# Optimization experiments

Measured on AMD Instinct MI355X. Metric: run time of the kernel, lower is better.

## Reference

```python
import jax, jax.numpy as jnp
import numpy as np

B, N, C = 8, 3072, 768
NUM_HEADS, NUM_DIL, KS = 12, 3, 3


def setup_inputs() -> dict:
    key = jax.random.key(0)
    k1, k2, k3 = jax.random.split(key, 3)
    x = jax.random.normal(k1, (B, N, C), dtype=jnp.float32)
    qkv_w = jax.random.normal(k2, (3 * C, C), dtype=jnp.float32) * 0.02
    proj_w = jax.random.normal(k3, (C, C), dtype=jnp.float32) * 0.02
    proj_b = jnp.zeros((C,), dtype=jnp.float32)
    return {"x": x, "qkv_w": qkv_w, "proj_w": proj_w, "proj_b": proj_b}


def reference(x, qkv_w, proj_w, proj_b):
    Bx, Nx, Cx = x.shape
    nd, ks, heads = NUM_DIL, KS, NUM_HEADS
    hd = Cx // heads          # head_dim = 64
    d = Cx // nd              # channels per dilation = 256
    h = heads // nd           # heads per dilation = 4
    nb = Nx // ks             # number of windows along N
    scale = hd ** -0.5

    # qkv: [B,N,3C] -> [nd,3,B,d,N] (matches torch permute(3,2,0,4,1))
    qkv = (x @ qkv_w.T).reshape(Bx, Nx, 3, nd, d)
    qkv = jnp.transpose(qkv, (3, 2, 0, 4, 1))
    q, k, v = qkv[:, 0], qkv[:, 1], qkv[:, 2]  # each [nd,B,d,N]

    def split_heads(t):
        # [nd,B,d,N] -> [nd,B,h,hd,ks,nb] -> [nd,B,h,nb,ks,hd]
        t = t.reshape(nd, Bx, h, hd, ks, nb)
        return jnp.transpose(t, (0, 1, 2, 5, 4, 3))

    qh = split_heads(q)
    kh = split_heads(k)
    vh = split_heads(v)

    # tiny per-window attention: [nd,B,h,nb,ks,ks]
    attn = jnp.einsum('nbhwqd,nbhwkd->nbhwqk', qh, kh) * scale
    attn = jax.nn.softmax(attn, axis=-1)
    out = jnp.einsum('nbhwqk,nbhwkd->nbhwqd', attn, vh)  # [nd,B,h,nb,ks,hd]

    # torch: transpose(1,2).reshape(B,N,d) per dilation, then permute(1,2,0,3).reshape(B,N,C)
    out = jnp.transpose(out, (0, 1, 3, 2, 4, 5)).reshape(nd, Bx, Nx, d)
    out = jnp.transpose(out, (1, 2, 0, 3)).reshape(Bx, Nx, Cx)
    return out @ proj_w.T + proj_b
```

## Files before the change

kernel.cpp:

```cpp
#include <hip/hip_runtime.h>
#include <stdint.h>

#define DEVFN __device__ __forceinline__

typedef unsigned short u16;
typedef __bf16 bf16_t;
typedef bf16_t bf16x8 __attribute__((ext_vector_type(8)));
typedef float  f32x4  __attribute__((ext_vector_type(4)));

static constexpr int Bb = 8, Nn = 3072, Cc = 768;
static constexpr int Mr = Bb * Nn;
static constexpr int C3 = 3 * Cc;
static constexpr int NB = 1024;

DEVFN u16 f2bf_rne(float f) {
  uint32_t u = __builtin_bit_cast(uint32_t, f);
  u += 0x7FFFu + ((u >> 16) & 1u);
  return (u16)(u >> 16);
}
DEVFN float bf2f(u16 v) {
  uint32_t u = ((uint32_t)v) << 16;
  return __builtin_bit_cast(float, u);
}

__global__ void cvt_all(const float4* __restrict__ x, const float4* __restrict__ wq,
                        const float4* __restrict__ wp, ushort4* __restrict__ xb,
                        ushort4* __restrict__ wqb, ushort4* __restrict__ wpb) {
  const int NX = Mr * Cc / 4, NQ = C3 * Cc / 4, NP = Cc * Cc / 4;
  int i = blockIdx.x * blockDim.x + threadIdx.x;
  const int stride = gridDim.x * blockDim.x;
  for (; i < NX + NQ + NP; i += stride) {
    const float4* src; ushort4* dst; int j;
    if (i < NX)           { src = x;  dst = xb;  j = i; }
    else if (i < NX + NQ) { src = wq; dst = wqb; j = i - NX; }
    else                  { src = wp; dst = wpb; j = i - NX - NQ; }
    float4 v = src[j];
    ushort4 o;
    o.x = f2bf_rne(v.x); o.y = f2bf_rne(v.y);
    o.z = f2bf_rne(v.z); o.w = f2bf_rne(v.w);
    dst[j] = o;
  }
}

DEVFN void gload_lds16(const void* g, void* l) {
  __builtin_amdgcn_global_load_lds(
      (const __attribute__((address_space(1))) uint32_t*)g,
      (__attribute__((address_space(3))) uint32_t*)l,
      16, 0, 0);
}

template <int BM, int BN, int WM, int WN, bool OUT_F32>
__global__ __launch_bounds__(WM * WN * 64, 2)
void gemm_bk64(const u16* __restrict__ A, const u16* __restrict__ Bw,
               void* __restrict__ Cout, const float* __restrict__ bias,
               int Ndim, int K) {
  constexpr int NT = WM * WN * 64;
  constexpr int MF = BM / WM / 16;
  constexpr int NF = BN / WN / 16;
  constexpr int SLOT = (BM + BN) * 128;
  static_assert(4 * (NT / 8) == BM && BM == BN, "staging geometry");
  __shared__ char lds[2 * SLOT];

  const int nTn = Ndim / BN;
  const int nwg = gridDim.x;
  const int bid = blockIdx.x;
  const int wgid = (bid & 7) * (nwg >> 3) + (bid >> 3);
  const int tm = wgid / nTn, tn = wgid % nTn;

  const int t = threadIdx.x;
  const int l = t & 63;
  const int w = t >> 6;
  const int wr = w / WN;
  const int wc = w % WN;

  const int NSL = K >> 6;

  const int srA = t >> 3;
  const int sw8 = ((t & 7) ^ ((t >> 3) & 7)) * 8;
  const u16* baseA = A  + (size_t)(tm * BM) * K + sw8;
  const u16* baseB = Bw + (size_t)(tn * BN) * K + sw8;

  const int lt0 = (l & 15) * 128 + (((l >> 4)    ) ^ (l & 7)) * 16;
  const int lt1 = (l & 15) * 128 + (((l >> 4) + 4) ^ (l & 7)) * 16;

  f32x4 acc[MF][NF];
  #pragma unroll
  for (int m = 0; m < MF; ++m)
    #pragma unroll
    for (int n = 0; n < NF; ++n)
      acc[m][n] = f32x4{0.f, 0.f, 0.f, 0.f};

#define STAGE(SL, P)                                                          \
  do {                                                                        \
    char* d = lds + (SL) * SLOT + t * 16;                                     \
    const size_t ko = (size_t)(P) * 64;                                       \
    _Pragma("unroll")                                                         \
    for (int k = 0; k < 4; ++k)                                               \
      gload_lds16(baseA + (size_t)(k * (NT / 8) + srA) * K + ko,              \
                  d + k * NT * 16);                                           \
    _Pragma("unroll")                                                         \
    for (int k = 0; k < 4; ++k)                                               \
      gload_lds16(baseB + (size_t)(k * (NT / 8) + srA) * K + ko,              \
                  d + (k + 4) * NT * 16);                                     \
  } while (0)

  STAGE(0, 0);

  for (int p = 0; p < NSL; ++p) {
    asm volatile("s_waitcnt vmcnt(0)" ::: "memory");
    __builtin_amdgcn_s_barrier();

    const char* ab = lds + (p & 1) * SLOT + wr * (BM / WM) * 128;
    const char* bb = lds + (p & 1) * SLOT + BM * 128 + wc * (BN / WN) * 128;

    bf16x8 af[MF], bf[NF];
    #pragma unroll
    for (int m = 0; m < MF; ++m)
      af[m] = *reinterpret_cast<const bf16x8*>(ab + m * 2048 + lt0);
    #pragma unroll
    for (int n = 0; n < NF; ++n)
      bf[n] = *reinterpret_cast<const bf16x8*>(bb + n * 2048 + lt0);

    if (p + 1 < NSL) STAGE((p + 1) & 1, p + 1);

    __builtin_amdgcn_s_setprio(1);
    #pragma unroll
    for (int m = 0; m < MF; ++m)
      #pragma unroll
      for (int n = 0; n < NF; ++n)
        acc[m][n] = __builtin_amdgcn_mfma_f32_16x16x32_bf16(bf[n], af[m],
                                                            acc[m][n], 0, 0, 0);
    __builtin_amdgcn_s_setprio(0);

    #pragma unroll
    for (int m = 0; m < MF; ++m)
      af[m] = *reinterpret_cast<const bf16x8*>(ab + m * 2048 + lt1);
    #pragma unroll
    for (int n = 0; n < NF; ++n)
      bf[n] = *reinterpret_cast<const bf16x8*>(bb + n * 2048 + lt1);

    __builtin_amdgcn_s_setprio(1);
    #pragma unroll
    for (int m = 0; m < MF; ++m)
      #pragma unroll
      for (int n = 0; n < NF; ++n)
        acc[m][n] = __builtin_amdgcn_mfma_f32_16x16x32_bf16(bf[n], af[m],
                                                            acc[m][n], 0, 0, 0);
    __builtin_amdgcn_s_setprio(0);
  }
#undef STAGE

  const int grow0 = tm * BM + wr * (BM / WM) + (l & 15);
  const int gcol0 = tn * BN + wc * (BN / WN) + (l >> 4) * 4;
  #pragma unroll
  for (int m = 0; m < MF; ++m) {
    const int row = grow0 + m * 16;
    #pragma unroll
    for (int n = 0; n < NF; ++n) {
      const int col = gcol0 + n * 16;
      if constexpr (OUT_F32) {
        float* O = (float*)Cout;
        const float4 bv = *reinterpret_cast<const float4*>(&bias[col]);
        float4 o;
        o.x = acc[m][n][0] + bv.x;
        o.y = acc[m][n][1] + bv.y;
        o.z = acc[m][n][2] + bv.z;
        o.w = acc[m][n][3] + bv.w;
        *reinterpret_cast<float4*>(&O[(size_t)row * Ndim + col]) = o;
      } else {
        u16* O = (u16*)Cout;
        ushort4 o;
        o.x = f2bf_rne(acc[m][n][0]);
        o.y = f2bf_rne(acc[m][n][1]);
        o.z = f2bf_rne(acc[m][n][2]);
        o.w = f2bf_rne(acc[m][n][3]);
        *reinterpret_cast<ushort4*>(&O[(size_t)row * Ndim + col]) = o;
      }
    }
  }
}

__global__ __launch_bounds__(256)
void attn_local4(const u16* __restrict__ qkv, u16* __restrict__ y) {
  const int t = threadIdx.x;
  const int l = t & 63;
  int wid = blockIdx.x * 4 + (t >> 6);
  const int w = wid & (NB - 1); wid >>= 10;
  const int b = wid & 7; wid >>= 3;
  const int dil = wid;

  const int colq = dil * 256 + l * 4;
  float q[3][4], k[3][4], v[3][4];
  #pragma unroll
  for (int i = 0; i < 3; ++i) {
    const size_t row = (size_t)(b * Nn + i * NB + w) * C3;
    const ushort4 q4 = *reinterpret_cast<const ushort4*>(&qkv[row + colq]);
    const ushort4 k4 = *reinterpret_cast<const ushort4*>(&qkv[row + 768 + colq]);
    const ushort4 v4 = *reinterpret_cast<const ushort4*>(&qkv[row + 1536 + colq]);
    q[i][0] = bf2f(q4.x); q[i][1] = bf2f(q4.y); q[i][2] = bf2f(q4.z); q[i][3] = bf2f(q4.w);
    k[i][0] = bf2f(k4.x); k[i][1] = bf2f(k4.y); k[i][2] = bf2f(k4.z); k[i][3] = bf2f(k4.w);
    v[i][0] = bf2f(v4.x); v[i][1] = bf2f(v4.y); v[i][2] = bf2f(v4.z); v[i][3] = bf2f(v4.w);
  }

  float s[3][3];
  #pragma unroll
  for (int i = 0; i < 3; ++i)
    #pragma unroll
    for (int j = 0; j < 3; ++j) {
      float p = q[i][0] * k[j][0] + q[i][1] * k[j][1]
              + q[i][2] * k[j][2] + q[i][3] * k[j][3];
      p += __shfl_xor(p, 1, 64);
      p += __shfl_xor(p, 2, 64);
      p += __shfl_xor(p, 4, 64);
      p += __shfl_xor(p, 8, 64);
      s[i][j] = p * 0.125f;
    }

  #pragma unroll
  for (int i = 0; i < 3; ++i) {
    const float mx = fmaxf(fmaxf(s[i][0], s[i][1]), s[i][2]);
    const float e0 = __expf(s[i][0] - mx);
    const float e1 = __expf(s[i][1] - mx);
    const float e2 = __expf(s[i][2] - mx);
    const float inv = 1.0f / (e0 + e1 + e2);
    ushort4 o4;
    u16* po = &o4.x;
    #pragma unroll
    for (int e = 0; e < 4; ++e)
      po[e] = f2bf_rne((e0 * v[0][e] + e1 * v[1][e] + e2 * v[2][e]) * inv);
    const int linear = (l >> 4) * 192 + i * 64 + (l & 15) * 4;
    const int nout = w * 3 + (linear >> 8);
    const int dd = linear & 255;
    *reinterpret_cast<ushort4*>(
        &y[(size_t)(b * Nn + nout) * Cc + dil * 256 + dd]) = o4;
  }
}

extern "C" void kernel_launch(void* const* d_in, const int* in_sizes, int n_in,
                              void* d_out, int out_size, void* d_ws, size_t ws_size,
                              hipStream_t stream) {
  const float* x      = (const float*)d_in[0];
  const float* qkv_w  = (const float*)d_in[1];
  const float* proj_w = (const float*)d_in[2];
  const float* proj_b = (const float*)d_in[3];

  char* ws = (char*)d_ws;
  u16* wq_b = (u16*)(ws);
  u16* wp_b = (u16*)(ws + 3538944);
  u16* xb   = (u16*)(ws + 4718592);
  u16* qkvb = (u16*)(ws + 42467328);
  u16* yb   = xb;

  cvt_all<<<2048, 256, 0, stream>>>((const float4*)x, (const float4*)qkv_w,
                                    (const float4*)proj_w, (ushort4*)xb,
                                    (ushort4*)wq_b, (ushort4*)wp_b);

  gemm_bk64<256, 256, 2, 4, false>
      <<<(Mr / 256) * (C3 / 256), 512, 0, stream>>>(xb, wq_b, qkvb, nullptr, C3, Cc);

  attn_local4<<<(3 * 8 * 1024) / 4, 256, 0, stream>>>(qkvb, yb);

  gemm_bk64<128, 128, 2, 2, true>
      <<<(Mr / 128) * (Cc / 128), 256, 0, stream>>>(yb, wp_b, d_out, proj_b, Cc, Cc);
}
```

Baseline: 203.2 us.

## Add 4-stage BK32 pipelined 256x256 GEMM for the QKV projection

Adds a dedicated 256x256-tile bf16 GEMM for the QKV projection. It uses K-steps of 32 with a 4-slot LDS ring, prefetching three phases ahead via global_load_lds and fine-grained vmcnt waits. It also uses a swizzled LDS layout and raises wave priority around the MFMA blocks. The goal is to hide global-load latency better than the previous double-buffered BK64 kernel. In exchange it uses 128KB of LDS, which may limit occupancy to one workgroup per CU despite the launch bound of 2.

After: 196.7 us, median of 2. -3.2%, faster.

```diff
diff --git a/kernel.cpp b/kernel.cpp
--- a/kernel.cpp
+++ b/kernel.cpp
@@ -47,6 +47,120 @@
       (const __attribute__((address_space(1))) uint32_t*)g,
       (__attribute__((address_space(3))) uint32_t*)l,
       16, 0, 0);
+}
+
+template <bool OUT_F32>
+__global__ __launch_bounds__(512, 2)
+void gemm256(const u16* __restrict__ A, const u16* __restrict__ Bw,
+             void* __restrict__ Cout, const float* __restrict__ bias,
+             int Ndim, int K) {
+  constexpr int SLOT = 32768;
+  __shared__ char lds[4 * SLOT];
+
+  const int nTn = Ndim >> 8;
+  const int nwg = gridDim.x;
+  const int bid = blockIdx.x;
+  const int wgid = (bid & 7) * (nwg >> 3) + (bid >> 3);
+  const int tm = wgid / nTn, tn = wgid % nTn;
+
+  const int t = threadIdx.x;
+  const int l = t & 63;
+  const int w = t >> 6;
+  const int wr = w >> 2;
+  const int wcq = w & 3;
+  const int lr = l & 15;
+
+  const int NPH = K >> 5;
+
+  const int srow = l >> 2;
+  const int scol = 8 * ((l & 3) ^ (srow & 3));
+  const u16* pA0 = A  + (size_t)(tm * 256 +       w * 16 + srow) * K + scol;
+  const u16* pA1 = A  + (size_t)(tm * 256 + 128 + w * 16 + srow) * K + scol;
+  const u16* pB0 = Bw + (size_t)(tn * 256 +       w * 16 + srow) * K + scol;
+  const u16* pB1 = Bw + (size_t)(tn * 256 + 128 + w * 16 + srow) * K + scol;
+
+  const int lane_off = lr * 64 + (((l >> 4) * 16) ^ ((lr & 3) << 4));
+
+  f32x4 acc[8][4];
+  #pragma unroll
+  for (int m = 0; m < 8; ++m)
+    #pragma unroll
+    for (int n = 0; n < 4; ++n)
+      acc[m][n] = f32x4{0.f, 0.f, 0.f, 0.f};
+
+  #pragma unroll
+  for (int q = 0; q < 3; ++q) {
+    char* dA = &lds[q * SLOT + w * 1024];
+    char* dB = &lds[q * SLOT + 16384 + w * 1024];
+    const size_t ko = (size_t)q * 32;
+    gload_lds16(pA0 + ko, dA);
+    gload_lds16(pA1 + ko, dA + 8192);
+    gload_lds16(pB0 + ko, dB);
+    gload_lds16(pB1 + ko, dB + 8192);
+  }
+
+#define GPHASE(VMSTR, PF_COND)                                                \
+  do {                                                                        \
+    asm volatile(VMSTR ::: "memory");                                         \
+    __builtin_amdgcn_s_barrier();                                             \
+    asm volatile("" ::: "memory");                                            \
+    const char* ab = &lds[(p & 3) * SLOT] + wr * 8192 + lane_off;             \
+    const char* bb = &lds[(p & 3) * SLOT + 16384] + wcq * 4096 + lane_off;    \
+    bf16x8 af[8], bf[4];                                                      \
+    _Pragma("unroll")                                                         \
+    for (int m = 0; m < 8; ++m)                                               \
+      af[m] = *reinterpret_cast<const bf16x8*>(ab + m * 1024);                \
+    _Pragma("unroll")                                                         \
+    for (int n = 0; n < 4; ++n)                                               \
+      bf[n] = *reinterpret_cast<const bf16x8*>(bb + n * 1024);                \
+    if (PF_COND) {                                                            \
+      const int ps = (p + 3) & 3;                                             \
+      char* dA = &lds[ps * SLOT + w * 1024];                                  \
+      char* dB = &lds[ps * SLOT + 16384 + w * 1024];                          \
+      const size_t ko = (size_t)(p + 3) * 32;                                 \
+      gload_lds16(pA0 + ko, dA);                                              \
+      gload_lds16(pA1 + ko, dA + 8192);                                       \
+      gload_lds16(pB0 + ko, dB);                                              \
+      gload_lds16(pB1 + ko, dB + 8192);                                       \
+    }                                                                         \
+    __builtin_amdgcn_s_setprio(1);                                            \
+    _Pragma("unroll")                                                         \
+    for (int m = 0; m < 8; ++m)                                               \
+      _Pragma("unroll")                                                       \
+      for (int n = 0; n < 4; ++n)                                             \
+        acc[m][n] = __builtin_amdgcn_mfma_f32_16x16x32_bf16(af[m], bf[n],     \
+                                                            acc[m][n], 0,0,0);\
+    __builtin_amdgcn_s_setprio(0);                                            \
+    asm volatile("" ::: "memory");                                            \
+  } while (0)
+
+  int p = 0;
+  for (; p < NPH - 2; ++p) GPHASE("s_waitcnt vmcnt(8)", (p + 3 < NPH));
+  GPHASE("s_waitcnt vmcnt(4)", false); ++p;
+  GPHASE("s_waitcnt vmcnt(0)", false); ++p;
+#undef GPHASE
+
+  const int rbase = tm * 256 + wr * 128 + (l >> 4) * 4;
+  #pragma unroll
+  for (int m = 0; m < 8; ++m) {
+    #pragma unroll
+    for (int n = 0; n < 4; ++n) {
+      const int col = tn * 256 + wcq * 64 + n * 16 + lr;
+      const int row0 = rbase + m * 16;
+      if constexpr (OUT_F32) {
+        float* O = (float*)Cout;
+        const float bv = bias[col];
+        #pragma unroll
+        for (int j = 0; j < 4; ++j)
+          O[(size_t)(row0 + j) * Ndim + col] = acc[m][n][j] + bv;
+      } else {
+        u16* O = (u16*)Cout;
+        #pragma unroll
+        for (int j = 0; j < 4; ++j)
+          O[(size_t)(row0 + j) * Ndim + col] = f2bf_rne(acc[m][n][j]);
+      }
+    }
+  }
 }
 
 template <int BM, int BN, int WM, int WN, bool OUT_F32>
@@ -255,8 +369,7 @@
                                     (const float4*)proj_w, (ushort4*)xb,
                                     (ushort4*)wq_b, (ushort4*)wp_b);
 
-  gemm_bk64<256, 256, 2, 4, false>
-      <<<(Mr / 256) * (C3 / 256), 512, 0, stream>>>(xb, wq_b, qkvb, nullptr, C3, Cc);
+  gemm256<false><<<(Mr / 256) * (C3 / 256), 512, 0, stream>>>(xb, wq_b, qkvb, nullptr, C3, Cc);
 
   attn_local4<<<(3 * 8 * 1024) / 4, 256, 0, stream>>>(qkvb, yb);
 
```
